# Kernel tuning notes

Measured on AMD Instinct MI355X. Metric: run time of the kernel, lower is better.

The kernel has to match this reference:

```python
import jax, jax.numpy as jnp
import numpy as np

B, T, C = 4, 2048, 1024
NH = 16
HD = C // NH


def setup_inputs() -> dict:
    key = jax.random.key(0)
    k1, k2, k3 = jax.random.split(key, 3)
    x = jax.random.normal(k1, (B, T, C), dtype=jnp.float32)
    Wqkv = jax.random.normal(k2, (C, 3 * C), dtype=jnp.float32) * 0.02
    bqkv = jnp.zeros((3 * C,), dtype=jnp.float32)
    Wproj = jax.random.normal(k3, (C, C), dtype=jnp.float32) * 0.02
    bproj = jnp.zeros((C,), dtype=jnp.float32)
    return {"x": x, "Wqkv": Wqkv, "bqkv": bqkv, "Wproj": Wproj, "bproj": bproj}


def reference(x, Wqkv, bqkv, Wproj, bproj):
    Bx, Tx, Cx = x.shape
    qkv = x @ Wqkv + bqkv  # [B,T,3C]
    q, k, v = jnp.split(qkv, 3, axis=-1)
    # [B, NH, T, HD]
    q = q.reshape(Bx, Tx, NH, HD).transpose(0, 2, 1, 3)
    k = k.reshape(Bx, Tx, NH, HD).transpose(0, 2, 1, 3)
    v = v.reshape(Bx, Tx, NH, HD).transpose(0, 2, 1, 3)
    scale = 1.0 / jnp.sqrt(jnp.float32(HD))
    att = jnp.einsum('bhqd,bhkd->bhqk', q, k) * scale  # [B,NH,T,T]
    causal = jnp.tril(jnp.ones((Tx, Tx), dtype=bool))
    att = jnp.where(causal, att, jnp.float32(-jnp.inf))
    att = jax.nn.softmax(att, axis=-1)
    y = jnp.einsum('bhqk,bhkd->bhqd', att, v)  # [B,NH,T,HD]
    y = y.transpose(0, 2, 1, 3).reshape(Bx, Tx, Cx)
    return y @ Wproj + bproj
```

## Files before the change

kernel.cpp:

```cpp
#include <hip/hip_runtime.h>
#include <hip/hip_bf16.h>
#include <math.h>

#define B_  4
#define T_  2048
#define C_  1024
#define NH_ 16
#define HD_ 64

using bf16 = __hip_bfloat16;
typedef __attribute__((ext_vector_type(8))) short bf16x8;
typedef __attribute__((ext_vector_type(4))) short bf16x4;
typedef __attribute__((ext_vector_type(4))) float f32x4;

__device__ __forceinline__ bf16 f2b(float f){ return __float2bfloat16(f); }

__device__ __forceinline__ short f2bs(float f){
  union { float f; unsigned u; } x; x.f = f;
  x.u += 0x7FFFu + ((x.u >> 16) & 1u);
  return (short)(x.u >> 16);
}

__device__ __forceinline__ bf16x4 pack_bf16x4(float a, float b, float c, float d){
  union { bf16x4 v; __hip_bfloat162 h[2]; } u;
  u.h[0] = __float22bfloat162_rn(make_float2(a, b));
  u.h[1] = __float22bfloat162_rn(make_float2(c, d));
  return u.v;
}

__device__ __forceinline__ void async_load16(const bf16* g, bf16* l){
  __builtin_amdgcn_global_load_lds((const __attribute__((address_space(1))) unsigned int*)g,
                                   (__attribute__((address_space(3))) unsigned int*)l,
                                   16, 0, 0);
}

#define QSCALE 0.18033688011112042f


__global__ __launch_bounds__(256) void k_cvt4(const float* __restrict__ in, bf16* __restrict__ out, int n){
  int i = (blockIdx.x * 256 + threadIdx.x) * 4;
  if (i < n){
    float4 f = *(const float4*)(in + i);
    ushort4 u;
    u.x = (unsigned short)f2bs(f.x);
    u.y = (unsigned short)f2bs(f.y);
    u.z = (unsigned short)f2bs(f.z);
    u.w = (unsigned short)f2bs(f.w);
    *(ushort4*)(out + i) = u;
  }
}

__global__ __launch_bounds__(256) void k_cvtT2(const float* __restrict__ in0, bf16* __restrict__ out0,
                                               const float* __restrict__ in1, bf16* __restrict__ out1){
  __shared__ float t[32][33];
  int b = blockIdx.x;
  const float* in; bf16* out; int Cc, bx, by;
  if (b < 3072){ in = in0; out = out0; Cc = 3*C_; bx = (b % 96)*32; by = (b / 96)*32; }
  else { b -= 3072; in = in1; out = out1; Cc = C_; bx = (b & 31)*32; by = (b >> 5)*32; }
  const int R = C_;
  int lx = threadIdx.x & 31, ly = threadIdx.x >> 5;
  #pragma unroll
  for (int s = 0; s < 4; s++){
    int k = by + ly + s*8;
    t[ly + s*8][lx] = in[(size_t)k * Cc + bx + lx];
  }
  __syncthreads();
  #pragma unroll
  for (int s = 0; s < 4; s++){
    int n = bx + ly + s*8;
    out[(size_t)n * R + by + lx] = f2b(t[lx][ly + s*8]);
  }
}

template<int MODE, int BM>
__global__ __launch_bounds__(BM*2) void k_gemm(
    const bf16* __restrict__ A, const bf16* __restrict__ BT,
    const float* __restrict__ bias,
    bf16* __restrict__ qo, bf16* __restrict__ ko, bf16* __restrict__ vo,
    float* __restrict__ fout,
    int M, int N, int K)
{
  constexpr int NTHR = BM*2;
  constexpr int WMW  = BM/64;
  constexpr int NB   = 512/NTHR;
  __shared__ bf16 As[2][BM*32];
  __shared__ bf16 Bs[2][128*32];

  const int tid  = threadIdx.x;
  const int wave = tid >> 6, lane = tid & 63;
  const int wm = wave % WMW, wn = wave / WMW;
  const int quad = lane >> 4, l15 = lane & 15;
  const int bm = blockIdx.x * BM;
  const int bn = blockIdx.y * 128;

  const bf16* gA[2]; bf16* lA[2];
  #pragma unroll
  for (int s = 0; s < 2; s++){
    const int c = tid + s*NTHR;
    const int r = c >> 2, p = (c & 3) ^ ((r >> 1) & 3);
    gA[s] = A + (size_t)(bm + r)*K + p*8;
    lA[s] = &As[0][0] + (size_t)c*8;
  }
  const bf16* gB[NB]; bf16* lB[NB];
  #pragma unroll
  for (int s = 0; s < NB; s++){
    const int c = tid + s*NTHR;
    const int r = c >> 2, p = (c & 3) ^ ((r >> 1) & 3);
    gB[s] = BT + (size_t)(bn + r)*K + p*8;
    lB[s] = &Bs[0][0] + (size_t)c*8;
  }
  const int fsw = (l15 >> 1) & 3;

  f32x4 acc[4][4] = {};
  const int nK = K >> 5;

  #pragma unroll
  for (int s = 0; s < 2; s++) async_load16(gA[s], lA[s]);
  #pragma unroll
  for (int s = 0; s < NB; s++) async_load16(gB[s], lB[s]);

  for (int kt = 0; kt < nK; kt++){
    __syncthreads();
    if (kt + 1 < nK){
      const int off = (kt + 1) * 32;
      const int ba  = ((kt + 1) & 1) * (BM*32);
      const int bb  = ((kt + 1) & 1) * 4096;
      #pragma unroll
      for (int s = 0; s < 2; s++) async_load16(gA[s] + off, lA[s] + ba);
      #pragma unroll
      for (int s = 0; s < NB; s++) async_load16(gB[s] + off, lB[s] + bb);
    }
    const bf16* as = &As[kt & 1][0];
    const bf16* bs = &Bs[kt & 1][0];

    bf16x8 af[4], bfv[4];
    #pragma unroll
    for (int i = 0; i < 4; i++)
      af[i]  = *reinterpret_cast<const bf16x8*>(as + (wm*64 + i*16 + l15)*32 + ((quad ^ fsw) << 3));
    #pragma unroll
    for (int j = 0; j < 4; j++)
      bfv[j] = *reinterpret_cast<const bf16x8*>(bs + (wn*64 + j*16 + l15)*32 + ((quad ^ fsw) << 3));
    #pragma unroll
    for (int i = 0; i < 4; i++)
      #pragma unroll
      for (int j = 0; j < 4; j++)
        acc[i][j] = __builtin_amdgcn_mfma_f32_16x16x32_bf16(af[i], bfv[j], acc[i][j], 0, 0, 0);
  }

  if (MODE == 0){
    const int sec = bn >> 10;
    const int bb2 = bm >> 11;
    const int tb  = (bm & (T_ - 1)) + wm*64 + quad*4;
    const int hn  = ((bn & 1023) >> 6) + wn;
    const size_t bhx = (size_t)(bb2 * NH_ + hn);
    if (sec == 2){
      #pragma unroll
      for (int j = 0; j < 4; j++){
        const int d = j*16 + l15;
        const float bj = bias[bn + wn*64 + j*16 + l15];
        bf16* vrow = vo + (bhx * HD_ + d) * (size_t)T_;
        const int sw = (l15 & 7) * 8;
        #pragma unroll
        for (int i = 0; i < 4; i++){
          const int t = (tb + i*16) ^ sw;
          *reinterpret_cast<bf16x4*>(vrow + t) =
            pack_bf16x4(acc[i][j][0] + bj, acc[i][j][1] + bj,
                        acc[i][j][2] + bj, acc[i][j][3] + bj);
        }
      }
    } else {
      bf16* dst = (sec == 0) ? qo : ko;
      const float sc = (sec == 0) ? QSCALE : 1.0f;
      #pragma unroll
      for (int j = 0; j < 4; j++){
        const int d = j*16 + l15;
        const float bj = bias[bn + wn*64 + j*16 + l15];
        bf16* base = dst + bhx * T_ * HD_;
        #pragma unroll
        for (int i = 0; i < 4; i++){
          const int t0 = tb + i*16;
          #pragma unroll
          for (int r = 0; r < 4; r++){
            const int dq = d ^ (((quad*4 + r) & 7) * 8);
            short s = f2bs((acc[i][j][r] + bj) * sc);
            base[(size_t)(t0 + r) * HD_ + dq] = *(bf16*)&s;
          }
        }
      }
    }
  } else {
    #pragma unroll
    for (int i = 0; i < 4; i++){
      #pragma unroll
      for (int j = 0; j < 4; j++){
        const int n = bn + wn*64 + j*16 + l15;
        const float bj = bias[n];
        float* p0 = fout + (size_t)(bm + wm*64 + i*16 + quad*4) * N + n;
        #pragma unroll
        for (int r = 0; r < 4; r++)
          p0[(size_t)r * N] = acc[i][j][r] + bj;
      }
    }
  }
}

__global__ __launch_bounds__(256) void k_attn(
    const bf16* __restrict__ Q, const bf16* __restrict__ Kg,
    const bf16* __restrict__ Vt, bf16* __restrict__ Y)
{
  __shared__ bf16 Ks[2][64*64];
  __shared__ bf16 Vs[2][64*64];

  const int bh = blockIdx.x;
  const int bb = bh >> 4, hh = bh & 15;
  const int tid  = threadIdx.x;
  const int wave = tid >> 6, lane = tid & 63;
  const int quad = lane >> 4, l15 = lane & 15;
  const int swz  = (l15 & 7) * 8;

  const size_t baseQK = (size_t)bh * T_ * HD_;
  const size_t baseV  = (size_t)bh * HD_ * T_;

  const int ca = wave, cb = wave + 4;
  const bf16* kg_a = Kg + baseQK + ca*512 + (size_t)lane*8;
  const bf16* kg_b = Kg + baseQK + cb*512 + (size_t)lane*8;
  const bf16* vg_a = Vt + baseV + (size_t)(ca*8 + (lane>>3)) * T_ + (lane&7)*8;
  const bf16* vg_b = Vt + baseV + (size_t)(cb*8 + (lane>>3)) * T_ + (lane&7)*8;
  bf16* kl_a0 = &Ks[0][0] + ca*512;  bf16* kl_b0 = &Ks[0][0] + cb*512;
  bf16* vl_a0 = &Vs[0][0] + ca*512;  bf16* vl_b0 = &Vs[0][0] + cb*512;

  bf16x4 ones_f;
  {
    short v = (l15 == 0) ? f2bs(1.0f) : (short)0;
    ones_f = (bf16x4){ v, v, v, v };
  }

  for (int phase = 0; phase < 2; phase++){
    const int qt = phase ? (31 - blockIdx.y) : blockIdx.y;
    const int jmax = qt;

    __syncthreads();

    bf16x8 qf[2];
    {
      const int t = qt*64 + wave*16 + l15;
      #pragma unroll
      for (int ks = 0; ks < 2; ks++){
        const int col = (ks*32 + quad*8) ^ swz;
        qf[ks] = *reinterpret_cast<const bf16x8*>(Q + baseQK + (size_t)t*HD_ + col);
      }
    }

    async_load16(kg_a, kl_a0);  async_load16(kg_b, kl_b0);
    async_load16(vg_a, vl_a0);  async_load16(vg_b, vl_b0);

    f32x4 o[5] = {};

    for (int j = 0; j <= jmax; j++){
      __syncthreads();

      if (j < jmax){
        const int nb = ((j+1) & 1) * 4096;
        const size_t ko = (size_t)(j+1) * 64 * HD_;
        async_load16(kg_a + ko, kl_a0 + nb);  async_load16(kg_b + ko, kl_b0 + nb);
        async_load16(vg_a + (j+1)*64, vl_a0 + nb);
        async_load16(vg_b + (j+1)*64, vl_b0 + nb);
      }

      const bf16* ksb = &Ks[j & 1][0];
      const bf16* vsb = &Vs[j & 1][0];

      f32x4 st[4] = {};
      #pragma unroll
      for (int ks = 0; ks < 2; ks++){
        #pragma unroll
        for (int tk = 0; tk < 4; tk++){
          bf16x8 kf = *reinterpret_cast<const bf16x8*>(ksb + (tk*16 + l15)*64 + ((ks*32 + quad*8) ^ swz));
          st[tk] = __builtin_amdgcn_mfma_f32_16x16x32_bf16(kf, qf[ks], st[tk], 0, 0, 0);
        }
      }

      const bool diag = (j == qt);
      bf16x4 pf[4];
      {
        const int qg = qt*64 + wave*16 + l15;
        #pragma unroll
        for (int tk = 0; tk < 4; tk++){
          float e[4];
          #pragma unroll
          for (int r = 0; r < 4; r++){
            float sv = st[tk][r];
            if (diag){
              const int kvg = j*64 + tk*16 + quad*4 + r;
              if (kvg > qg) sv = -1e30f;
            }
            e[r] = exp2f(sv);
          }
          pf[tk] = pack_bf16x4(e[0], e[1], e[2], e[3]);
        }
      }

      #pragma unroll
      for (int td = 0; td < 4; td++){
        #pragma unroll
        for (int tk = 0; tk < 4; tk++){
          bf16x4 vf = *reinterpret_cast<const bf16x4*>(vsb + (td*16 + l15)*64 + ((tk*16 + quad*4) ^ swz));
          o[td] = __builtin_amdgcn_mfma_f32_16x16x16bf16_1k(vf, pf[tk], o[td], 0, 0, 0);
        }
      }
      #pragma unroll
      for (int tk = 0; tk < 4; tk++)
        o[4] = __builtin_amdgcn_mfma_f32_16x16x16bf16_1k(ones_f, pf[tk], o[4], 0, 0, 0);
    }

    {
      const float l = __shfl(o[4][0], l15, 64);
      const float inv = 1.0f / l;
      const int t = qt*64 + wave*16 + l15;
      bf16* yrow = Y + ((size_t)(bb * T_ + t)) * C_ + hh * HD_;
      #pragma unroll
      for (int td = 0; td < 4; td++){
        *reinterpret_cast<bf16x4*>(yrow + td*16 + quad*4) =
          pack_bf16x4(o[td][0] * inv, o[td][1] * inv,
                      o[td][2] * inv, o[td][3] * inv);
      }
    }
  }
}


extern "C" void kernel_launch(void* const* d_in, const int* in_sizes, int n_in,
                              void* d_out, int out_size, void* d_ws, size_t ws_size,
                              hipStream_t stream) {
  const float* x     = (const float*)d_in[0];
  const float* Wqkv  = (const float*)d_in[1];
  const float* bqkv  = (const float*)d_in[2];
  const float* Wproj = (const float*)d_in[3];
  const float* bproj = (const float*)d_in[4];
  float* out = (float*)d_out;

  const size_t M = (size_t)B_ * T_;
  char* w = (char*)d_ws;
  bf16* xb     = (bf16*)w;  w += M * C_ * 2;
  bf16* WqkvT  = (bf16*)w;  w += (size_t)3 * C_ * C_ * 2;
  bf16* WprojT = (bf16*)w;  w += (size_t)C_ * C_ * 2;
  bf16* Qb     = (bf16*)w;  w += M * C_ * 2;
  bf16* Kb     = (bf16*)w;  w += M * C_ * 2;
  bf16* Vtb    = (bf16*)w;  w += M * C_ * 2;
  bf16* Yb     = (bf16*)w;  w += M * C_ * 2;

  {
    int n = (int)(M * C_);
    k_cvt4<<<dim3((n/4 + 255)/256), dim3(256), 0, stream>>>(x, xb, n);
  }
  k_cvtT2<<<dim3(4096), dim3(256), 0, stream>>>(Wqkv, WqkvT, Wproj, WprojT);
  k_gemm<0,256><<<dim3(M/256, (3*C_)/128), dim3(512), 0, stream>>>(
      xb, WqkvT, bqkv, Qb, Kb, Vtb, nullptr, (int)M, 3*C_, C_);
  k_attn<<<dim3(64, 16), dim3(256), 0, stream>>>(Qb, Kb, Vtb, Yb);
  k_gemm<1,128><<<dim3(M/128, C_/128), dim3(256), 0, stream>>>(
      Yb, WprojT, bproj, nullptr, nullptr, nullptr, out, (int)M, C_, C_);
}
```

Baseline: 260.3 us.

## Process 128-query tiles per block to reuse K/V tiles across two query sub-tiles

Result: no change. 258.5 us (-0.7%).

```diff
diff --git a/kernel.cpp b/kernel.cpp
--- a/kernel.cpp
+++ b/kernel.cpp
@@ -213,6 +213,7 @@
 
   const int bh = blockIdx.x;
   const int bb = bh >> 4, hh = bh & 15;
+  const int qt = 15 - blockIdx.y;
   const int tid  = threadIdx.x;
   const int wave = tid >> 6, lane = tid & 63;
   const int quad = lane >> 4, l15 = lane & 15;
@@ -235,95 +236,101 @@
     ones_f = (bf16x4){ v, v, v, v };
   }
 
-  for (int phase = 0; phase < 2; phase++){
-    const int qt = phase ? (31 - blockIdx.y) : blockIdx.y;
-    const int jmax = qt;
-
+  const int jmax = 2*qt + 1;
+
+  bf16x8 qf[2][2];
+  #pragma unroll
+  for (int s = 0; s < 2; s++){
+    const int t = qt*128 + s*64 + wave*16 + l15;
+    #pragma unroll
+    for (int ks = 0; ks < 2; ks++){
+      const int col = (ks*32 + quad*8) ^ swz;
+      qf[s][ks] = *reinterpret_cast<const bf16x8*>(Q + baseQK + (size_t)t*HD_ + col);
+    }
+  }
+
+  async_load16(kg_a, kl_a0);  async_load16(kg_b, kl_b0);
+  async_load16(vg_a, vl_a0);  async_load16(vg_b, vl_b0);
+
+  f32x4 o[2][5] = {};
+
+  for (int j = 0; j <= jmax; j++){
     __syncthreads();
 
-    bf16x8 qf[2];
-    {
-      const int t = qt*64 + wave*16 + l15;
-      #pragma unroll
-      for (int ks = 0; ks < 2; ks++){
-        const int col = (ks*32 + quad*8) ^ swz;
-        qf[ks] = *reinterpret_cast<const bf16x8*>(Q + baseQK + (size_t)t*HD_ + col);
-      }
-    }
-
-    async_load16(kg_a, kl_a0);  async_load16(kg_b, kl_b0);
-    async_load16(vg_a, vl_a0);  async_load16(vg_b, vl_b0);
-
-    f32x4 o[5] = {};
-
-    for (int j = 0; j <= jmax; j++){
-      __syncthreads();
-
-      if (j < jmax){
-        const int nb = ((j+1) & 1) * 4096;
-        const size_t ko = (size_t)(j+1) * 64 * HD_;
-        async_load16(kg_a + ko, kl_a0 + nb);  async_load16(kg_b + ko, kl_b0 + nb);
-        async_load16(vg_a + (j+1)*64, vl_a0 + nb);
-        async_load16(vg_b + (j+1)*64, vl_b0 + nb);
-      }
-
-      const bf16* ksb = &Ks[j & 1][0];
-      const bf16* vsb = &Vs[j & 1][0];
-
-      f32x4 st[4] = {};
-      #pragma unroll
-      for (int ks = 0; ks < 2; ks++){
+    if (j < jmax){
+      const int nb = ((j+1) & 1) * 4096;
+      const size_t ko = (size_t)(j+1) * 64 * HD_;
+      async_load16(kg_a + ko, kl_a0 + nb);  async_load16(kg_b + ko, kl_b0 + nb);
+      async_load16(vg_a + (j+1)*64, vl_a0 + nb);
+      async_load16(vg_b + (j+1)*64, vl_b0 + nb);
+    }
+
+    const bf16* ksb = &Ks[j & 1][0];
+    const bf16* vsb = &Vs[j & 1][0];
+
+    f32x4 st[2][4] = {};
+    __builtin_amdgcn_s_setprio(1);
+    #pragma unroll
+    for (int ks = 0; ks < 2; ks++){
+      #pragma unroll
+      for (int tk = 0; tk < 4; tk++){
+        bf16x8 kf = *reinterpret_cast<const bf16x8*>(ksb + (tk*16 + l15)*64 + ((ks*32 + quad*8) ^ swz));
+        st[0][tk] = __builtin_amdgcn_mfma_f32_16x16x32_bf16(kf, qf[0][ks], st[0][tk], 0, 0, 0);
+        st[1][tk] = __builtin_amdgcn_mfma_f32_16x16x32_bf16(kf, qf[1][ks], st[1][tk], 0, 0, 0);
+      }
+    }
+    __builtin_amdgcn_s_setprio(0);
+
+    bf16x4 pf[2][4];
+    #pragma unroll
+    for (int s = 0; s < 2; s++){
+      const int qg = qt*128 + s*64 + wave*16 + l15;
+      const bool msk = s ? (j > 2*qt) : (j >= 2*qt);
+      #pragma unroll
+      for (int tk = 0; tk < 4; tk++){
+        float e[4];
         #pragma unroll
-        for (int tk = 0; tk < 4; tk++){
-          bf16x8 kf = *reinterpret_cast<const bf16x8*>(ksb + (tk*16 + l15)*64 + ((ks*32 + quad*8) ^ swz));
-          st[tk] = __builtin_amdgcn_mfma_f32_16x16x32_bf16(kf, qf[ks], st[tk], 0, 0, 0);
+        for (int r = 0; r < 4; r++){
+          float sv = st[s][tk][r];
+          if (msk){
+            const int kvg = j*64 + tk*16 + quad*4 + r;
+            if (kvg > qg) sv = -1e30f;
+          }
+          e[r] = exp2f(sv);
         }
-      }
-
-      const bool diag = (j == qt);
-      bf16x4 pf[4];
-      {
-        const int qg = qt*64 + wave*16 + l15;
-        #pragma unroll
-        for (int tk = 0; tk < 4; tk++){
-          float e[4];
-          #pragma unroll
-          for (int r = 0; r < 4; r++){
-            float sv = st[tk][r];
-            if (diag){
-              const int kvg = j*64 + tk*16 + quad*4 + r;
-              if (kvg > qg) sv = -1e30f;
-            }
-            e[r] = exp2f(sv);
-          }
-          pf[tk] = pack_bf16x4(e[0], e[1], e[2], e[3]);
-        }
-      }
-
-      #pragma unroll
-      for (int td = 0; td < 4; td++){
-        #pragma unroll
-        for (int tk = 0; tk < 4; tk++){
-          bf16x4 vf = *reinterpret_cast<const bf16x4*>(vsb + (td*16 + l15)*64 + ((tk*16 + quad*4) ^ swz));
-          o[td] = __builtin_amdgcn_mfma_f32_16x16x16bf16_1k(vf, pf[tk], o[td], 0, 0, 0);
-        }
-      }
-      #pragma unroll
-      for (int tk = 0; tk < 4; tk++)
-        o[4] = __builtin_amdgcn_mfma_f32_16x16x16bf16_1k(ones_f, pf[tk], o[4], 0, 0, 0);
-    }
-
-    {
-      const float l = __shfl(o[4][0], l15, 64);
-      const float inv = 1.0f / l;
-      const int t = qt*64 + wave*16 + l15;
-      bf16* yrow = Y + ((size_t)(bb * T_ + t)) * C_ + hh * HD_;
-      #pragma unroll
-      for (int td = 0; td < 4; td++){
-        *reinterpret_cast<bf16x4*>(yrow + td*16 + quad*4) =
-          pack_bf16x4(o[td][0] * inv, o[td][1] * inv,
-                      o[td][2] * inv, o[td][3] * inv);
-      }
+        pf[s][tk] = pack_bf16x4(e[0], e[1], e[2], e[3]);
+      }
+    }
+
+    __builtin_amdgcn_s_setprio(1);
+    #pragma unroll
+    for (int td = 0; td < 4; td++){
+      #pragma unroll
+      for (int tk = 0; tk < 4; tk++){
+        bf16x4 vf = *reinterpret_cast<const bf16x4*>(vsb + (td*16 + l15)*64 + ((tk*16 + quad*4) ^ swz));
+        o[0][td] = __builtin_amdgcn_mfma_f32_16x16x16bf16_1k(vf, pf[0][tk], o[0][td], 0, 0, 0);
+        o[1][td] = __builtin_amdgcn_mfma_f32_16x16x16bf16_1k(vf, pf[1][tk], o[1][td], 0, 0, 0);
+      }
+    }
+    #pragma unroll
+    for (int tk = 0; tk < 4; tk++){
+      o[0][4] = __builtin_amdgcn_mfma_f32_16x16x16bf16_1k(ones_f, pf[0][tk], o[0][4], 0, 0, 0);
+      o[1][4] = __builtin_amdgcn_mfma_f32_16x16x16bf16_1k(ones_f, pf[1][tk], o[1][4], 0, 0, 0);
+    }
+    __builtin_amdgcn_s_setprio(0);
+  }
+
+  #pragma unroll
+  for (int s = 0; s < 2; s++){
+    const float l = __shfl(o[s][4][0], l15, 64);
+    const float inv = 1.0f / l;
+    const int t = qt*128 + s*64 + wave*16 + l15;
+    bf16* yrow = Y + ((size_t)(bb * T_ + t)) * C_ + hh * HD_;
+    #pragma unroll
+    for (int td = 0; td < 4; td++){
+      *reinterpret_cast<bf16x4*>(yrow + td*16 + quad*4) =
+        pack_bf16x4(o[s][td][0] * inv, o[s][td][1] * inv,
+                    o[s][td][2] * inv, o[s][td][3] * inv);
     }
   }
 }
```
